# Performance work log

Measured on AMD Instinct MI355X. Metric: run time of the kernel, lower is better.

## Reference

```python
import jax, jax.numpy as jnp
import numpy as np

H = 128          # input hidden dim
HID = 128        # expert hidden width
OUT = 128        # out_channels
NR = 8           # n_routed
NS = 2           # n_shared
RDIM = 16        # router feature dim


def setup_inputs() -> dict:
    key = jax.random.key(0)
    ks = jax.random.split(key, 11)
    s = 0.05
    x = jax.random.normal(ks[0], (2, 32, 32, 32, H), dtype=jnp.float32)
    # router params
    Wr1 = jax.random.normal(ks[1], (H, RDIM), dtype=jnp.float32) * s
    br1 = jnp.zeros((RDIM,), dtype=jnp.float32)
    Wr2 = jax.random.normal(ks[2], (RDIM, NR), dtype=jnp.float32) * s
    br2 = jnp.zeros((NR,), dtype=jnp.float32)
    # routed expert params, stacked on leading expert axis
    We1 = jax.random.normal(ks[3], (NR, H, HID), dtype=jnp.float32) * s
    be1 = jnp.zeros((NR, HID), dtype=jnp.float32)
    We2 = jax.random.normal(ks[4], (NR, HID, OUT), dtype=jnp.float32) * s
    be2 = jnp.zeros((NR, OUT), dtype=jnp.float32)
    # shared expert params
    Ws1 = jax.random.normal(ks[5], (NS, H, HID), dtype=jnp.float32) * s
    bs1 = jnp.zeros((NS, HID), dtype=jnp.float32)
    Ws2 = jax.random.normal(ks[6], (NS, HID, OUT), dtype=jnp.float32) * s
    bs2 = jnp.zeros((NS, OUT), dtype=jnp.float32)
    return dict(x=x, Wr1=Wr1, br1=br1, Wr2=Wr2, br2=br2,
                We1=We1, be1=be1, We2=We2, be2=be2,
                Ws1=Ws1, bs1=bs1, Ws2=Ws2, bs2=bs2)


def reference(x, Wr1, br1, Wr2, br2, We1, be1, We2, be2, Ws1, bs1, Ws2, bs2):
    # router: Dense(16) -> relu -> Dense(n_routed) -> softmax
    rf = jax.nn.relu(jnp.einsum('...h,hr->...r', x, Wr1) + br1)
    logits = jnp.einsum('...r,re->...e', rf, Wr2) + br2
    gate = jax.nn.softmax(logits, axis=-1)                      # [..., NR]
    threshold = 1.0 / NR
    mask = (gate > threshold).astype(gate.dtype)
    mg = gate * mask
    mg = mg / (jnp.sum(mg, axis=-1, keepdims=True) + 1e-8)
    # routed experts (batched over expert axis e): Dense -> gelu(tanh) -> Dense
    hr = jax.nn.gelu(jnp.einsum('...h,ehd->...ed', x, We1) + be1)   # [..., NR, HID]
    ro = jnp.einsum('...ed,edo->...eo', hr, We2) + be2              # [..., NR, OUT]
    routed_agg = jnp.einsum('...eo,...e->...o', ro, mg)
    # shared experts summed
    hs = jax.nn.gelu(jnp.einsum('...h,ehd->...ed', x, Ws1) + bs1)   # [..., NS, HID]
    so = jnp.einsum('...ed,edo->...eo', hs, Ws2) + bs2              # [..., NS, OUT]
    shared_agg = jnp.sum(so, axis=-2)
    return routed_agg + shared_agg
```

## Files before the change

kernel.cpp:

```cpp
#include <hip/hip_runtime.h>
#include <hip/hip_bf16.h>

typedef __bf16 bf16x8 __attribute__((ext_vector_type(8)));
typedef float  f32x16 __attribute__((ext_vector_type(16)));
typedef float  f32x4  __attribute__((ext_vector_type(4)));
typedef float  f32x2  __attribute__((ext_vector_type(2)));

static __device__ __forceinline__ f32x16 mfma32(bf16x8 a, bf16x8 b, f32x16 c) {
    return __builtin_amdgcn_mfma_f32_32x32x16_bf16(a, b, c, 0, 0, 0);
}

#define GELU_C1 2.30220820f
#define GELU_C2 0.10294324f

static __device__ __forceinline__ bf16x8 gelu8(f32x16 a, int base, float gv) {
    bf16x8 r;
    #pragma unroll
    for (int p = 0; p < 4; ++p) {
        f32x2 hh; hh[0] = a[base + 2 * p]; hh[1] = a[base + 2 * p + 1];
        f32x2 tt = hh * hh;
        f32x2 pp;
        pp[0] = fmaf(tt[0], -GELU_C2, -GELU_C1);
        pp[1] = fmaf(tt[1], -GELU_C2, -GELU_C1);
        f32x2 mm = hh * pp;
        float e0 = __builtin_amdgcn_exp2f(mm[0]);
        float e1 = __builtin_amdgcn_exp2f(mm[1]);
        float q0 = __builtin_amdgcn_rcpf(1.f + e0);
        float q1 = __builtin_amdgcn_rcpf(1.f + e1);
        r[2 * p]     = (__bf16)(hh[0] * q0 * gv);
        r[2 * p + 1] = (__bf16)(hh[1] * q1 * gv);
    }
    return r;
}

__global__ __launch_bounds__(256) void pack_kernel(
    const float* __restrict__ We1, const float* __restrict__ be1,
    const float* __restrict__ Ws1, const float* __restrict__ bs1,
    const float* __restrict__ We2, const float* __restrict__ Ws2,
    const float* __restrict__ Wr1, const float* __restrict__ br1,
    const float* __restrict__ Wr2, const float* __restrict__ br2,
    __bf16* __restrict__ w1p, __bf16* __restrict__ w2p,
    float* __restrict__ be1p,
    double* __restrict__ wr1d, double* __restrict__ br1d,
    double* __restrict__ wr2d, double* __restrict__ br2d)
{
    int tid = blockIdx.x * 256 + threadIdx.x;
    if (tid < 20480) {
        int l  = tid & 63;
        int ks = (tid >> 6) & 7;
        int nt = (tid >> 9) & 3;
        int e  = tid >> 11;
        const float* src = (e < 8) ? (We1 + e * 16384) : (Ws1 + (e - 8) * 16384);
        int n  = nt * 32 + (l & 31);
        int kb = ks * 16 + (l >> 5) * 8;
        bf16x8 v;
        #pragma unroll
        for (int j = 0; j < 8; ++j) v[j] = (__bf16)src[(kb + j) * 128 + n];
        *(bf16x8*)(w1p + (size_t)tid * 8) = v;
    } else if (tid < 40960) {
        int t2 = tid - 20480;
        int l  = t2 & 63;
        int ks = (t2 >> 6) & 7;
        int ot = (t2 / 512) & 3;
        int e  = t2 / 2048;
        const float* src = (e < 8) ? (We2 + e * 16384) : (Ws2 + (e - 8) * 16384);
        int o  = ot * 32 + (l & 31);
        int lh = l >> 5;
        bf16x8 v;
        #pragma unroll
        for (int j = 0; j < 8; ++j) {
            int hid = 16 * ks + 8 * (j >> 2) + 4 * lh + (j & 3);
            v[j] = (__bf16)src[hid * 128 + o];
        }
        *(bf16x8*)(w2p + (size_t)t2 * 8) = v;
    } else if (tid < 42240) {
        int i  = tid - 40960;
        int r  = i & 15;
        int h2 = (i >> 4) & 1;
        int nt = (i >> 5) & 3;
        int e  = i >> 7;
        int n  = 32 * nt + (r & 3) + 8 * (r >> 2) + 4 * h2;
        be1p[i] = (e < 8) ? be1[e * 128 + n] : bs1[(e - 8) * 128 + n];
    } else if (tid < 44288) {
        int i = tid - 42240;
        wr1d[i] = (double)Wr1[i];
    } else if (tid < 44416) {
        int i = tid - 44288;
        wr2d[i] = (double)Wr2[i];
    } else if (tid < 44432) {
        int i = tid - 44416;
        br1d[i] = (double)br1[i];
    } else if (tid < 44440) {
        int i = tid - 44432;
        br2d[i] = (double)br2[i];
    }
}

__global__ __launch_bounds__(256, 2) void moe_main_kernel(
    const float* __restrict__ x,
    const double* __restrict__ wr1d, const double* __restrict__ br1d,
    const double* __restrict__ wr2d, const double* __restrict__ br2d,
    const __bf16* __restrict__ w1p, const __bf16* __restrict__ w2p,
    const float* __restrict__ be1p,
    const float* __restrict__ be2, const float* __restrict__ bs2,
    float* __restrict__ out)
{
    __shared__ __align__(16) char lds[69632];
    __bf16* Xp  = (__bf16*)lds;
    __bf16* Hs  = (__bf16*)(lds + 32768);
    float*  mg  = (float*)(lds + 65536);
    double* rfs = (double*)(lds + 32768);

    const int t    = threadIdx.x;
    const int lane = t & 63;
    const int wave = t >> 6;
    const int l31  = lane & 31;
    const int hi   = lane >> 5;
    const int mp   = wave >> 1;
    const int oh   = wave & 1;
    const int tok0 = blockIdx.x * 128;

    const bf16x8* w1v = (const bf16x8*)w1p;
    const bf16x8* w2v = (const bf16x8*)w2p;

    bf16x8 wb0[8], wb1[8], wB0[8];
    {
        const bf16x8* wp  = w1v + ((size_t)(2 * oh) * 8) * 64 + lane;
        const bf16x8* wBp = w2v + ((size_t)(2 * oh) * 8) * 64 + lane;
        #pragma unroll
        for (int ks = 0; ks < 8; ++ks) {
            wb0[ks] = wp[ks * 64];
            wb1[ks] = wp[(8 + ks) * 64];
            wB0[ks] = wBp[ks * 64];
        }
    }

    #pragma unroll
    for (int i = 0; i < 8; ++i) {
        int g = i * 256 + t;
        int m = g >> 4;
        int c = g & 15;
        const f32x4* sp = (const f32x4*)(x + (size_t)(tok0 + m) * 128 + c * 8);
        f32x4 va = sp[0], vb = sp[1];
        bf16x8 v;
        v[0]=(__bf16)va[0]; v[1]=(__bf16)va[1]; v[2]=(__bf16)va[2]; v[3]=(__bf16)va[3];
        v[4]=(__bf16)vb[0]; v[5]=(__bf16)vb[1]; v[6]=(__bf16)vb[2]; v[7]=(__bf16)vb[3];
        *(bf16x8*)&Xp[(((m >> 5) * 8 + (c >> 1)) * 64 + (c & 1) * 32 + (m & 31)) * 8] = v;
    }

    {
        const int tok = t >> 1;
        const int rq8 = (t & 1) * 8;
        double rf[8];
        #pragma unroll
        for (int j = 0; j < 8; ++j) rf[j] = br1d[rq8 + j];
        const float* xr = x + (size_t)(tok0 + tok) * 128;
        #pragma unroll 4
        for (int c = 0; c < 64; ++c) {
            f32x2 xv2 = *(const f32x2*)(xr + c * 2);
            #pragma unroll
            for (int q = 0; q < 2; ++q) {
                double xv = (double)xv2[q];
                const double* wrow = wr1d + (c * 2 + q) * 16 + rq8;
                #pragma unroll
                for (int j = 0; j < 8; ++j) rf[j] = fma(xv, wrow[j], rf[j]);
            }
        }
        double* rr = rfs + tok * 17 + rq8;
        #pragma unroll
        for (int j = 0; j < 8; ++j) rr[j] = rf[j] > 0.0 ? rf[j] : 0.0;
    }
    __syncthreads();

    if (t < 128) {
        double lg[8];
        #pragma unroll
        for (int j = 0; j < 8; ++j) lg[j] = br2d[j];
        #pragma unroll
        for (int r = 0; r < 16; ++r) {
            double rv = rfs[t * 17 + r];
            #pragma unroll
            for (int j = 0; j < 8; ++j)
                lg[j] = fma(rv, wr2d[r * 8 + j], lg[j]);
        }
        double mx = lg[0];
        #pragma unroll
        for (int j = 1; j < 8; ++j) mx = lg[j] > mx ? lg[j] : mx;
        double ex[8]; double s = 0.0;
        #pragma unroll
        for (int j = 0; j < 8; ++j) { ex[j] = exp(lg[j] - mx); s += ex[j]; }
        double ms = 0.0;
        bool mk[8];
        #pragma unroll
        for (int j = 0; j < 8; ++j) {
            mk[j] = (8.0 * ex[j] > s);
            ms += mk[j] ? ex[j] : 0.0;
        }
        double inv = 1.0 / (ms + s * 1e-8);
        f32x4 o0, o1;
        #pragma unroll
        for (int j = 0; j < 4; ++j) {
            o0[j] = mk[j]     ? (float)(ex[j] * inv)     : 0.f;
            o1[j] = mk[4 + j] ? (float)(ex[4 + j] * inv) : 0.f;
        }
        *(f32x4*)&mg[t * 8]     = o0;
        *(f32x4*)&mg[t * 8 + 4] = o1;
    }
    __syncthreads();

    f32x16 acc00, acc01, acc10, acc11;
    #pragma unroll
    for (int i = 0; i < 16; ++i) { acc00[i]=0.f; acc01[i]=0.f; acc10[i]=0.f; acc11[i]=0.f; }

    #pragma unroll 1
    for (int e = 0; e < 10; ++e) {
        float gv0 = 1.0f, gv1 = 1.0f;
        if (e < 8) {
            gv0 = mg[(64 * mp + l31) * 8 + e];
            gv1 = mg[(64 * mp + 32 + l31) * 8 + e];
        }
        const float* bp = be1p + (size_t)((e * 4 + 2 * oh) * 2 + hi) * 16;
        f32x16 bA = *(const f32x16*)bp;
        f32x16 bB = *(const f32x16*)(bp + 32);

        __builtin_amdgcn_s_setprio(1);
        f32x16 a0, a1;
        #pragma unroll
        for (int i = 0; i < 16; ++i) { a0[i] = 0.f; a1[i] = 0.f; }
        #pragma unroll
        for (int ks = 0; ks < 8; ++ks) {
            bf16x8 xb = *(const bf16x8*)&Xp[(((2 * mp) * 8 + ks) * 64 + lane) * 8];
            a0 = mfma32(wb0[ks], xb, a0);
            a1 = mfma32(wb1[ks], xb, a1);
        }
        __builtin_amdgcn_s_setprio(0);
        a0 += bA; a1 += bB;
        {
            int rb = ((2 * mp) * 8 + 4 * oh) * 64 + lane;
            *(bf16x8*)&Hs[(rb + 0 * 64) * 8] = gelu8(a0, 0, gv0);
            *(bf16x8*)&Hs[(rb + 1 * 64) * 8] = gelu8(a0, 8, gv0);
            *(bf16x8*)&Hs[(rb + 2 * 64) * 8] = gelu8(a1, 0, gv0);
            *(bf16x8*)&Hs[(rb + 3 * 64) * 8] = gelu8(a1, 8, gv0);
        }
        __builtin_amdgcn_s_setprio(1);
        f32x16 c0, c1;
        #pragma unroll
        for (int i = 0; i < 16; ++i) { c0[i] = 0.f; c1[i] = 0.f; }
        #pragma unroll
        for (int ks = 0; ks < 8; ++ks) {
            bf16x8 xb = *(const bf16x8*)&Xp[(((2 * mp + 1) * 8 + ks) * 64 + lane) * 8];
            c0 = mfma32(wb0[ks], xb, c0);
            c1 = mfma32(wb1[ks], xb, c1);
        }
        __builtin_amdgcn_s_setprio(0);
        if (e < 9) {
            const bf16x8* wp = w1v + ((size_t)((e + 1) * 4 + 2 * oh) * 8) * 64 + lane;
            #pragma unroll
            for (int ks = 0; ks < 8; ++ks) {
                wb0[ks] = wp[ks * 64];
                wb1[ks] = wp[(8 + ks) * 64];
            }
        }
        c0 += bA; c1 += bB;
        {
            int rb = ((2 * mp + 1) * 8 + 4 * oh) * 64 + lane;
            *(bf16x8*)&Hs[(rb + 0 * 64) * 8] = gelu8(c0, 0, gv1);
            *(bf16x8*)&Hs[(rb + 1 * 64) * 8] = gelu8(c0, 8, gv1);
            *(bf16x8*)&Hs[(rb + 2 * 64) * 8] = gelu8(c1, 0, gv1);
            *(bf16x8*)&Hs[(rb + 3 * 64) * 8] = gelu8(c1, 8, gv1);
        }
        __syncthreads();

        bf16x8 wB1[8];
        {
            const bf16x8* wBp = w2v + ((size_t)(e * 4 + 2 * oh) * 8) * 64 + lane;
            #pragma unroll
            for (int kq = 0; kq < 8; ++kq) wB1[kq] = wBp[(8 + kq) * 64];
        }
        __builtin_amdgcn_s_setprio(1);
        #pragma unroll
        for (int kq = 0; kq < 8; ++kq) {
            bf16x8 h0 = *(const bf16x8*)&Hs[(((2 * mp)     * 8 + kq) * 64 + lane) * 8];
            bf16x8 h1 = *(const bf16x8*)&Hs[(((2 * mp + 1) * 8 + kq) * 64 + lane) * 8];
            acc00 = mfma32(h0, wB0[kq], acc00);
            acc01 = mfma32(h0, wB1[kq], acc01);
            acc10 = mfma32(h1, wB0[kq], acc10);
            acc11 = mfma32(h1, wB1[kq], acc11);
        }
        __builtin_amdgcn_s_setprio(0);
        if (e < 9) {
            const bf16x8* wBn = w2v + ((size_t)((e + 1) * 4 + 2 * oh) * 8) * 64 + lane;
            #pragma unroll
            for (int kq = 0; kq < 8; ++kq) wB0[kq] = wBn[kq * 64];
        }
        __syncthreads();
    }

    {
        float be2c[2][8], bsc[2];
        #pragma unroll
        for (int oti = 0; oti < 2; ++oti) {
            int o = 32 * (2 * oh + oti) + l31;
            bsc[oti] = bs2[o] + bs2[128 + o];
            #pragma unroll
            for (int ee = 0; ee < 8; ++ee) be2c[oti][ee] = be2[ee * 128 + o];
        }
        #pragma unroll
        for (int mi = 0; mi < 2; ++mi) {
            const int mt = 2 * mp + mi;
            const float* mgb = mg + (32 * mt) * 8;
            f32x16 aA = mi ? acc10 : acc00;
            f32x16 aB = mi ? acc11 : acc01;
            #pragma unroll
            for (int r = 0; r < 16; ++r) {
                int mrow = (r & 3) + 8 * (r >> 2) + 4 * hi;
                f32x4 g0 = *(const f32x4*)&mgb[mrow * 8];
                f32x4 g1 = *(const f32x4*)&mgb[mrow * 8 + 4];
                size_t orow = (size_t)(tok0 + 32 * mt + mrow) * 128;
                float b0 = bsc[0], b1 = bsc[1];
                #pragma unroll
                for (int ee = 0; ee < 4; ++ee) {
                    b0 = fmaf(g0[ee], be2c[0][ee], b0);
                    b1 = fmaf(g0[ee], be2c[1][ee], b1);
                }
                #pragma unroll
                for (int ee = 0; ee < 4; ++ee) {
                    b0 = fmaf(g1[ee], be2c[0][4 + ee], b0);
                    b1 = fmaf(g1[ee], be2c[1][4 + ee], b1);
                }
                out[orow + 32 * (2 * oh)     + l31] = aA[r] + b0;
                out[orow + 32 * (2 * oh + 1) + l31] = aB[r] + b1;
            }
        }
    }
}

extern "C" void kernel_launch(void* const* d_in, const int* in_sizes, int n_in,
                              void* d_out, int out_size, void* d_ws, size_t ws_size,
                              hipStream_t stream)
{
    const float* x   = (const float*)d_in[0];
    const float* Wr1 = (const float*)d_in[1];
    const float* br1 = (const float*)d_in[2];
    const float* Wr2 = (const float*)d_in[3];
    const float* br2 = (const float*)d_in[4];
    const float* We1 = (const float*)d_in[5];
    const float* be1 = (const float*)d_in[6];
    const float* We2 = (const float*)d_in[7];
    const float* be2 = (const float*)d_in[8];
    const float* Ws1 = (const float*)d_in[9];
    const float* bs1 = (const float*)d_in[10];
    const float* Ws2 = (const float*)d_in[11];
    const float* bs2 = (const float*)d_in[12];

    __bf16* w1p  = (__bf16*)d_ws;
    __bf16* w2p  = (__bf16*)((char*)d_ws + 327680);
    float*  be1p = (float*)((char*)d_ws + 655360);
    double* wr1d = (double*)((char*)d_ws + 660480);
    double* wr2d = (double*)((char*)d_ws + 676864);
    double* br1d = (double*)((char*)d_ws + 677888);
    double* br2d = (double*)((char*)d_ws + 678016);

    pack_kernel<<<174, 256, 0, stream>>>(We1, be1, Ws1, bs1, We2, Ws2,
                                         Wr1, br1, Wr2, br2,
                                         w1p, w2p, be1p, wr1d, br1d, wr2d, br2d);
    moe_main_kernel<<<512, 256, 0, stream>>>(x, wr1d, br1d, wr2d, br2d,
                                             w1p, w2p, be1p, be2, bs2,
                                             (float*)d_out);
}
```

Before: 200.6 us.

## Split router into separate kernel and keep per-wave hidden tiles in registers

Moves the fp64 router and gating into a separate kernel that writes gates to workspace. The main kernel then gives each wave its own 32-token tile. The first GEMM's output fragments are fed straight as A operands into the second GEMM, so the LDS staging of X and H and the block-wide barriers are gone. The W2 packing layout is reordered to match, and weight fragments are double-buffered per hidden tile. This adds a kernel launch and a global round trip for the gates, and each wave now loads the full weight set itself, which raises weight traffic through L2.

```diff
diff --git a/kernel.cpp b/kernel.cpp
--- a/kernel.cpp
+++ b/kernel.cpp
@@ -60,16 +60,16 @@
     } else if (tid < 40960) {
         int t2 = tid - 20480;
         int l  = t2 & 63;
-        int ks = (t2 >> 6) & 7;
-        int ot = (t2 / 512) & 3;
-        int e  = t2 / 2048;
+        int ot = (t2 >> 6) & 3;
+        int kq = (t2 >> 8) & 7;
+        int e  = t2 >> 11;
         const float* src = (e < 8) ? (We2 + e * 16384) : (Ws2 + (e - 8) * 16384);
-        int o  = ot * 32 + (l & 31);
+        int o  = 32 * ot + (l & 31);
         int lh = l >> 5;
         bf16x8 v;
         #pragma unroll
         for (int j = 0; j < 8; ++j) {
-            int hid = 16 * ks + 8 * (j >> 2) + 4 * lh + (j & 3);
+            int hid = 16 * kq + 8 * (j >> 2) + 4 * lh + (j & 3);
             v[j] = (__bf16)src[hid * 128 + o];
         }
         *(bf16x8*)(w2p + (size_t)t2 * 8) = v;
@@ -96,240 +96,224 @@
     }
 }
 
-__global__ __launch_bounds__(256, 2) void moe_main_kernel(
+__global__ __launch_bounds__(256) void router_kernel(
     const float* __restrict__ x,
     const double* __restrict__ wr1d, const double* __restrict__ br1d,
     const double* __restrict__ wr2d, const double* __restrict__ br2d,
+    float* __restrict__ gates)
+{
+    __shared__ __align__(16) char lds[41472];
+    float*  xs  = (float*)lds;
+    double* rfs = (double*)(lds + 33280);
+
+    const int t    = threadIdx.x;
+    const int tok0 = blockIdx.x * 64;
+
+    #pragma unroll
+    for (int i = 0; i < 8; ++i) {
+        int cid = i * 256 + t;
+        int m = cid >> 5;
+        int c = cid & 31;
+        f32x4 v = *(const f32x4*)(x + (size_t)(tok0 + m) * 128 + c * 4);
+        f32x2 s0, s1;
+        s0[0] = v[0]; s0[1] = v[1]; s1[0] = v[2]; s1[1] = v[3];
+        *(f32x2*)(xs + m * 130 + c * 4)     = s0;
+        *(f32x2*)(xs + m * 130 + c * 4 + 2) = s1;
+    }
+    __syncthreads();
+
+    {
+        const int tok = t & 63;
+        const int rq  = (t >> 6) * 4;
+        const int rqs = __builtin_amdgcn_readfirstlane(rq);
+        double rf4[4];
+        #pragma unroll
+        for (int j = 0; j < 4; ++j) rf4[j] = br1d[rqs + j];
+        const float* xr = xs + tok * 130;
+        #pragma unroll 4
+        for (int c = 0; c < 64; ++c) {
+            f32x2 xv2 = *(const f32x2*)(xr + c * 2);
+            #pragma unroll
+            for (int q = 0; q < 2; ++q) {
+                double xv = (double)xv2[q];
+                int k = c * 2 + q;
+                #pragma unroll
+                for (int j = 0; j < 4; ++j)
+                    rf4[j] = fma(xv, wr1d[k * 16 + rqs + j], rf4[j]);
+            }
+        }
+        #pragma unroll
+        for (int j = 0; j < 4; ++j)
+            rfs[tok * 16 + rq + j] = rf4[j] > 0.0 ? rf4[j] : 0.0;
+    }
+    __syncthreads();
+
+    if (t < 64) {
+        double lg[8];
+        #pragma unroll
+        for (int j = 0; j < 8; ++j) lg[j] = br2d[j];
+        #pragma unroll
+        for (int r = 0; r < 16; ++r) {
+            double rv = rfs[t * 16 + r];
+            #pragma unroll
+            for (int j = 0; j < 8; ++j)
+                lg[j] = fma(rv, wr2d[r * 8 + j], lg[j]);
+        }
+        double mx = lg[0];
+        #pragma unroll
+        for (int j = 1; j < 8; ++j) mx = lg[j] > mx ? lg[j] : mx;
+        double ex[8]; double s = 0.0;
+        #pragma unroll
+        for (int j = 0; j < 8; ++j) { ex[j] = exp(lg[j] - mx); s += ex[j]; }
+        double ms = 0.0;
+        bool mk[8];
+        #pragma unroll
+        for (int j = 0; j < 8; ++j) {
+            mk[j] = (8.0 * ex[j] > s);
+            ms += mk[j] ? ex[j] : 0.0;
+        }
+        double inv = 1.0 / (ms + s * 1e-8);
+        f32x4 o0, o1;
+        #pragma unroll
+        for (int j = 0; j < 4; ++j) {
+            o0[j] = mk[j]     ? (float)(ex[j] * inv)     : 0.f;
+            o1[j] = mk[4 + j] ? (float)(ex[4 + j] * inv) : 0.f;
+        }
+        *(f32x4*)(gates + (size_t)(tok0 + t) * 8)     = o0;
+        *(f32x4*)(gates + (size_t)(tok0 + t) * 8 + 4) = o1;
+    }
+}
+
+#define GEMM2_STEP(W)                                   \
+    acc0 = mfma32(h0, W[0], acc0);                      \
+    acc1 = mfma32(h0, W[1], acc1);                      \
+    acc2 = mfma32(h0, W[2], acc2);                      \
+    acc3 = mfma32(h0, W[3], acc3);                      \
+    acc0 = mfma32(h1, W[4], acc0);                      \
+    acc1 = mfma32(h1, W[5], acc1);                      \
+    acc2 = mfma32(h1, W[6], acc2);                      \
+    acc3 = mfma32(h1, W[7], acc3);
+
+#define PREF_WB(W, en, ntn)                                                  \
+    {                                                                        \
+        const bf16x8* bp2 = w2v + ((size_t)((en) * 32 + 8 * (ntn))) * 64 + lane; \
+        _Pragma("unroll")                                                    \
+        for (int f = 0; f < 8; ++f) W[f] = bp2[f * 64];                      \
+    }
+
+__global__ __launch_bounds__(256, 2) void moe_main_kernel(
+    const float* __restrict__ x, const float* __restrict__ gates,
     const __bf16* __restrict__ w1p, const __bf16* __restrict__ w2p,
     const float* __restrict__ be1p,
     const float* __restrict__ be2, const float* __restrict__ bs2,
     float* __restrict__ out)
 {
-    __shared__ __align__(16) char lds[69632];
-    __bf16* Xp  = (__bf16*)lds;
-    __bf16* Hs  = (__bf16*)(lds + 32768);
-    float*  mg  = (float*)(lds + 65536);
-    double* rfs = (double*)(lds + 32768);
-
     const int t    = threadIdx.x;
     const int lane = t & 63;
-    const int wave = t >> 6;
+    const int mt   = t >> 6;
     const int l31  = lane & 31;
     const int hi   = lane >> 5;
-    const int mp   = wave >> 1;
-    const int oh   = wave & 1;
     const int tok0 = blockIdx.x * 128;
+    const size_t row = (size_t)(tok0 + 32 * mt + l31);
 
     const bf16x8* w1v = (const bf16x8*)w1p;
     const bf16x8* w2v = (const bf16x8*)w2p;
 
-    bf16x8 wb0[8], wb1[8], wB0[8];
+    bf16x8 wb[8];
     {
-        const bf16x8* wp  = w1v + ((size_t)(2 * oh) * 8) * 64 + lane;
-        const bf16x8* wBp = w2v + ((size_t)(2 * oh) * 8) * 64 + lane;
+        const bf16x8* wp = w1v + lane;
+        #pragma unroll
+        for (int ks = 0; ks < 8; ++ks) wb[ks] = wp[ks * 64];
+    }
+    bf16x8 wBa[8], wBb[8];
+    PREF_WB(wBa, 0, 0)
+
+    bf16x8 xf[8];
+    {
+        const float* xr = x + row * 128 + 8 * hi;
         #pragma unroll
         for (int ks = 0; ks < 8; ++ks) {
-            wb0[ks] = wp[ks * 64];
-            wb1[ks] = wp[(8 + ks) * 64];
-            wB0[ks] = wBp[ks * 64];
-        }
-    }
-
+            f32x4 va = *(const f32x4*)(xr + 16 * ks);
+            f32x4 vb = *(const f32x4*)(xr + 16 * ks + 4);
+            bf16x8 v;
+            v[0]=(__bf16)va[0]; v[1]=(__bf16)va[1]; v[2]=(__bf16)va[2]; v[3]=(__bf16)va[3];
+            v[4]=(__bf16)vb[0]; v[5]=(__bf16)vb[1]; v[6]=(__bf16)vb[2]; v[7]=(__bf16)vb[3];
+            xf[ks] = v;
+        }
+    }
+
+    f32x16 acc0, acc1, acc2, acc3;
     #pragma unroll
-    for (int i = 0; i < 8; ++i) {
-        int g = i * 256 + t;
-        int m = g >> 4;
-        int c = g & 15;
-        const f32x4* sp = (const f32x4*)(x + (size_t)(tok0 + m) * 128 + c * 8);
-        f32x4 va = sp[0], vb = sp[1];
-        bf16x8 v;
-        v[0]=(__bf16)va[0]; v[1]=(__bf16)va[1]; v[2]=(__bf16)va[2]; v[3]=(__bf16)va[3];
-        v[4]=(__bf16)vb[0]; v[5]=(__bf16)vb[1]; v[6]=(__bf16)vb[2]; v[7]=(__bf16)vb[3];
-        *(bf16x8*)&Xp[(((m >> 5) * 8 + (c >> 1)) * 64 + (c & 1) * 32 + (m & 31)) * 8] = v;
-    }
-
-    {
-        const int tok = t >> 1;
-        const int rq8 = (t & 1) * 8;
-        double rf[8];
-        #pragma unroll
-        for (int j = 0; j < 8; ++j) rf[j] = br1d[rq8 + j];
-        const float* xr = x + (size_t)(tok0 + tok) * 128;
-        #pragma unroll 4
-        for (int c = 0; c < 64; ++c) {
-            f32x2 xv2 = *(const f32x2*)(xr + c * 2);
-            #pragma unroll
-            for (int q = 0; q < 2; ++q) {
-                double xv = (double)xv2[q];
-                const double* wrow = wr1d + (c * 2 + q) * 16 + rq8;
-                #pragma unroll
-                for (int j = 0; j < 8; ++j) rf[j] = fma(xv, wrow[j], rf[j]);
-            }
-        }
-        double* rr = rfs + tok * 17 + rq8;
-        #pragma unroll
-        for (int j = 0; j < 8; ++j) rr[j] = rf[j] > 0.0 ? rf[j] : 0.0;
-    }
-    __syncthreads();
-
-    if (t < 128) {
-        double lg[8];
-        #pragma unroll
-        for (int j = 0; j < 8; ++j) lg[j] = br2d[j];
-        #pragma unroll
-        for (int r = 0; r < 16; ++r) {
-            double rv = rfs[t * 17 + r];
-            #pragma unroll
-            for (int j = 0; j < 8; ++j)
-                lg[j] = fma(rv, wr2d[r * 8 + j], lg[j]);
-        }
-        double mx = lg[0];
-        #pragma unroll
-        for (int j = 1; j < 8; ++j) mx = lg[j] > mx ? lg[j] : mx;
-        double ex[8]; double s = 0.0;
-        #pragma unroll
-        for (int j = 0; j < 8; ++j) { ex[j] = exp(lg[j] - mx); s += ex[j]; }
-        double ms = 0.0;
-        bool mk[8];
-        #pragma unroll
-        for (int j = 0; j < 8; ++j) {
-            mk[j] = (8.0 * ex[j] > s);
-            ms += mk[j] ? ex[j] : 0.0;
-        }
-        double inv = 1.0 / (ms + s * 1e-8);
-        f32x4 o0, o1;
-        #pragma unroll
-        for (int j = 0; j < 4; ++j) {
-            o0[j] = mk[j]     ? (float)(ex[j] * inv)     : 0.f;
-            o1[j] = mk[4 + j] ? (float)(ex[4 + j] * inv) : 0.f;
-        }
-        *(f32x4*)&mg[t * 8]     = o0;
-        *(f32x4*)&mg[t * 8 + 4] = o1;
-    }
-    __syncthreads();
-
-    f32x16 acc00, acc01, acc10, acc11;
-    #pragma unroll
-    for (int i = 0; i < 16; ++i) { acc00[i]=0.f; acc01[i]=0.f; acc10[i]=0.f; acc11[i]=0.f; }
+    for (int i = 0; i < 16; ++i) { acc0[i]=0.f; acc1[i]=0.f; acc2[i]=0.f; acc3[i]=0.f; }
 
     #pragma unroll 1
     for (int e = 0; e < 10; ++e) {
-        float gv0 = 1.0f, gv1 = 1.0f;
-        if (e < 8) {
-            gv0 = mg[(64 * mp + l31) * 8 + e];
-            gv1 = mg[(64 * mp + 32 + l31) * 8 + e];
-        }
-        const float* bp = be1p + (size_t)((e * 4 + 2 * oh) * 2 + hi) * 16;
-        f32x16 bA = *(const f32x16*)bp;
-        f32x16 bB = *(const f32x16*)(bp + 32);
-
-        __builtin_amdgcn_s_setprio(1);
-        f32x16 a0, a1;
-        #pragma unroll
-        for (int i = 0; i < 16; ++i) { a0[i] = 0.f; a1[i] = 0.f; }
-        #pragma unroll
-        for (int ks = 0; ks < 8; ++ks) {
-            bf16x8 xb = *(const bf16x8*)&Xp[(((2 * mp) * 8 + ks) * 64 + lane) * 8];
-            a0 = mfma32(wb0[ks], xb, a0);
-            a1 = mfma32(wb1[ks], xb, a1);
-        }
-        __builtin_amdgcn_s_setprio(0);
-        a0 += bA; a1 += bB;
-        {
-            int rb = ((2 * mp) * 8 + 4 * oh) * 64 + lane;
-            *(bf16x8*)&Hs[(rb + 0 * 64) * 8] = gelu8(a0, 0, gv0);
-            *(bf16x8*)&Hs[(rb + 1 * 64) * 8] = gelu8(a0, 8, gv0);
-            *(bf16x8*)&Hs[(rb + 2 * 64) * 8] = gelu8(a1, 0, gv0);
-            *(bf16x8*)&Hs[(rb + 3 * 64) * 8] = gelu8(a1, 8, gv0);
-        }
-        __builtin_amdgcn_s_setprio(1);
-        f32x16 c0, c1;
-        #pragma unroll
-        for (int i = 0; i < 16; ++i) { c0[i] = 0.f; c1[i] = 0.f; }
-        #pragma unroll
-        for (int ks = 0; ks < 8; ++ks) {
-            bf16x8 xb = *(const bf16x8*)&Xp[(((2 * mp + 1) * 8 + ks) * 64 + lane) * 8];
-            c0 = mfma32(wb0[ks], xb, c0);
-            c1 = mfma32(wb1[ks], xb, c1);
-        }
-        __builtin_amdgcn_s_setprio(0);
-        if (e < 9) {
-            const bf16x8* wp = w1v + ((size_t)((e + 1) * 4 + 2 * oh) * 8) * 64 + lane;
-            #pragma unroll
-            for (int ks = 0; ks < 8; ++ks) {
-                wb0[ks] = wp[ks * 64];
-                wb1[ks] = wp[(8 + ks) * 64];
+        float gv = 1.0f;
+        if (e < 8) gv = gates[row * 8 + e];
+
+        #pragma unroll
+        for (int nt = 0; nt < 4; ++nt) {
+            const f32x16 bfr = *(const f32x16*)(be1p + ((e * 4 + nt) * 2 + hi) * 16);
+
+            __builtin_amdgcn_s_setprio(1);
+            f32x16 a;
+            #pragma unroll
+            for (int i = 0; i < 16; ++i) a[i] = 0.f;
+            #pragma unroll
+            for (int ks = 0; ks < 8; ++ks) a = mfma32(wb[ks], xf[ks], a);
+            __builtin_amdgcn_s_setprio(0);
+
+            {
+                int en  = (nt == 3) ? (e < 9 ? e + 1 : 9) : e;
+                int ntn = (nt + 1) & 3;
+                const bf16x8* wp = w1v + ((size_t)(en * 4 + ntn) * 8) * 64 + lane;
+                #pragma unroll
+                for (int ks = 0; ks < 8; ++ks) wb[ks] = wp[ks * 64];
             }
-        }
-        c0 += bA; c1 += bB;
-        {
-            int rb = ((2 * mp + 1) * 8 + 4 * oh) * 64 + lane;
-            *(bf16x8*)&Hs[(rb + 0 * 64) * 8] = gelu8(c0, 0, gv1);
-            *(bf16x8*)&Hs[(rb + 1 * 64) * 8] = gelu8(c0, 8, gv1);
-            *(bf16x8*)&Hs[(rb + 2 * 64) * 8] = gelu8(c1, 0, gv1);
-            *(bf16x8*)&Hs[(rb + 3 * 64) * 8] = gelu8(c1, 8, gv1);
-        }
-        __syncthreads();
-
-        bf16x8 wB1[8];
-        {
-            const bf16x8* wBp = w2v + ((size_t)(e * 4 + 2 * oh) * 8) * 64 + lane;
-            #pragma unroll
-            for (int kq = 0; kq < 8; ++kq) wB1[kq] = wBp[(8 + kq) * 64];
-        }
-        __builtin_amdgcn_s_setprio(1);
-        #pragma unroll
-        for (int kq = 0; kq < 8; ++kq) {
-            bf16x8 h0 = *(const bf16x8*)&Hs[(((2 * mp)     * 8 + kq) * 64 + lane) * 8];
-            bf16x8 h1 = *(const bf16x8*)&Hs[(((2 * mp + 1) * 8 + kq) * 64 + lane) * 8];
-            acc00 = mfma32(h0, wB0[kq], acc00);
-            acc01 = mfma32(h0, wB1[kq], acc01);
-            acc10 = mfma32(h1, wB0[kq], acc10);
-            acc11 = mfma32(h1, wB1[kq], acc11);
-        }
-        __builtin_amdgcn_s_setprio(0);
-        if (e < 9) {
-            const bf16x8* wBn = w2v + ((size_t)((e + 1) * 4 + 2 * oh) * 8) * 64 + lane;
-            #pragma unroll
-            for (int kq = 0; kq < 8; ++kq) wB0[kq] = wBn[kq * 64];
-        }
-        __syncthreads();
+
+            a += bfr;
+            bf16x8 h0 = gelu8(a, 0, gv);
+            bf16x8 h1 = gelu8(a, 8, gv);
+
+            __builtin_amdgcn_s_setprio(1);
+            if ((nt & 1) == 0) { GEMM2_STEP(wBa) } else { GEMM2_STEP(wBb) }
+            __builtin_amdgcn_s_setprio(0);
+
+            {
+                int en  = (nt == 3) ? (e < 9 ? e + 1 : 9) : e;
+                int ntn = (nt + 1) & 3;
+                if ((nt & 1) == 0) { PREF_WB(wBb, en, ntn) }
+                else               { PREF_WB(wBa, en, ntn) }
+            }
+        }
     }
 
     {
-        float be2c[2][8], bsc[2];
-        #pragma unroll
-        for (int oti = 0; oti < 2; ++oti) {
-            int o = 32 * (2 * oh + oti) + l31;
-            bsc[oti] = bs2[o] + bs2[128 + o];
-            #pragma unroll
-            for (int ee = 0; ee < 8; ++ee) be2c[oti][ee] = be2[ee * 128 + o];
-        }
-        #pragma unroll
-        for (int mi = 0; mi < 2; ++mi) {
-            const int mt = 2 * mp + mi;
-            const float* mgb = mg + (32 * mt) * 8;
-            f32x16 aA = mi ? acc10 : acc00;
-            f32x16 aB = mi ? acc11 : acc01;
-            #pragma unroll
-            for (int r = 0; r < 16; ++r) {
-                int mrow = (r & 3) + 8 * (r >> 2) + 4 * hi;
-                f32x4 g0 = *(const f32x4*)&mgb[mrow * 8];
-                f32x4 g1 = *(const f32x4*)&mgb[mrow * 8 + 4];
-                size_t orow = (size_t)(tok0 + 32 * mt + mrow) * 128;
-                float b0 = bsc[0], b1 = bsc[1];
+        float be2c[4][8], bsc[4];
+        #pragma unroll
+        for (int ot = 0; ot < 4; ++ot) {
+            int o = 32 * ot + l31;
+            bsc[ot] = bs2[o] + bs2[128 + o];
+            #pragma unroll
+            for (int ee = 0; ee < 8; ++ee) be2c[ot][ee] = be2[ee * 128 + o];
+        }
+        #pragma unroll
+        for (int r = 0; r < 16; ++r) {
+            int mrow = (r & 3) + 8 * (r >> 2) + 4 * hi;
+            size_t trow = (size_t)(tok0 + 32 * mt + mrow);
+            f32x4 g0 = *(const f32x4*)(gates + trow * 8);
+            f32x4 g1 = *(const f32x4*)(gates + trow * 8 + 4);
+            size_t obase = trow * 128 + l31;
+            #pragma unroll
+            for (int ot = 0; ot < 4; ++ot) {
+                float b = bsc[ot];
                 #pragma unroll
-                for (int ee = 0; ee < 4; ++ee) {
-                    b0 = fmaf(g0[ee], be2c[0][ee], b0);
-                    b1 = fmaf(g0[ee], be2c[1][ee], b1);
-                }
+                for (int ee = 0; ee < 4; ++ee) b = fmaf(g0[ee], be2c[ot][ee], b);
                 #pragma unroll
-                for (int ee = 0; ee < 4; ++ee) {
-                    b0 = fmaf(g1[ee], be2c[0][4 + ee], b0);
-                    b1 = fmaf(g1[ee], be2c[1][4 + ee], b1);
-                }
-                out[orow + 32 * (2 * oh)     + l31] = aA[r] + b0;
-                out[orow + 32 * (2 * oh + 1) + l31] = aB[r] + b1;
+                for (int ee = 0; ee < 4; ++ee) b = fmaf(g1[ee], be2c[ot][4 + ee], b);
+                float av = (ot == 0) ? acc0[r] : (ot == 1) ? acc1[r]
+                         : (ot == 2) ? acc2[r] : acc3[r];
+                out[obase + 32 * ot] = av + b;
             }
         }
     }
@@ -360,11 +344,12 @@
     double* wr2d = (double*)((char*)d_ws + 676864);
     double* br1d = (double*)((char*)d_ws + 677888);
     double* br2d = (double*)((char*)d_ws + 678016);
+    float*  gts  = (float*)((char*)d_ws + 720896);
 
     pack_kernel<<<174, 256, 0, stream>>>(We1, be1, Ws1, bs1, We2, Ws2,
                                          Wr1, br1, Wr2, br2,
                                          w1p, w2p, be1p, wr1d, br1d, wr2d, br2d);
-    moe_main_kernel<<<512, 256, 0, stream>>>(x, wr1d, br1d, wr2d, br2d,
-                                             w1p, w2p, be1p, be2, bs2,
+    router_kernel<<<1024, 256, 0, stream>>>(x, wr1d, br1d, wr2d, br2d, gts);
+    moe_main_kernel<<<512, 256, 0, stream>>>(x, gts, w1p, w2p, be1p, be2, bs2,
                                              (float*)d_out);
 }
```

Result: faster. 182.4 us (-9.1%).
